# Performance work log

Measured on AMD Instinct MI355X. Metric: run time of the kernel, lower is better.

The kernel has to match this reference:

```python
import jax, jax.numpy as jnp
import numpy as np

B, N, D = 2, 512, 64
LN_EPS = 1e-5
NEG_SLOPE = 0.01  # torch nn.LeakyReLU default


def _layer_norm(x, g, b):
    m = jnp.mean(x, axis=-1, keepdims=True)
    v = jnp.mean(jnp.square(x - m), axis=-1, keepdims=True)
    return (x - m) * jax.lax.rsqrt(v + LN_EPS) * g + b


def setup_inputs() -> dict:
    key = jax.random.key(0)
    k0, k1, k2 = jax.random.split(key, 3)
    return {
        "ua": jax.random.normal(k0, (B, N, D), dtype=jnp.float32),
        "iid": jax.random.normal(k1, (B, 1, 1, D), dtype=jnp.float32),
        "ln_g": jnp.ones((D,), dtype=jnp.float32),
        "ln_b": jnp.zeros((D,), dtype=jnp.float32),
        "w_att": (jax.random.normal(k2, (3 * D, 1), dtype=jnp.float32)
                  / np.sqrt(3 * D).astype(np.float32)),
        "b_att": jnp.zeros((1,), dtype=jnp.float32),
    }


def reference(ua, iid, ln_g, ln_b, w_att, b_att):
    b, n, d = ua.shape
    # all-pairs expand: query[b,i,j,:] = ua[b,i,:], key[b,i,j,:] = ua[b,j,:]
    query = jnp.broadcast_to(ua[:, :, None, :], (b, n, n, d))
    key = jnp.broadcast_to(ua[:, None, :, :], (b, n, n, d))
    value = query * key
    iid_e = jnp.broadcast_to(iid, (b, n, n, d))
    wq = _layer_norm(query, ln_g, ln_b)
    wk = _layer_norm(key, ln_g, ln_b)
    wiid = _layer_norm(iid_e, ln_g, ln_b)
    qk = jnp.concatenate((wq, wk, wiid), axis=-1)  # [b,n,n,3d]
    qk = qk @ w_att + b_att                        # [b,n,n,1]
    qk = jax.nn.leaky_relu(qk, NEG_SLOPE)
    # dropout in eval mode -> identity
    scores = jnp.squeeze(qk, axis=-1)              # [b,n,n]
    alphas = jax.nn.softmax(scores, axis=-1)       # softmax over keys j
    alphas = jnp.broadcast_to(alphas[..., None], value.shape)
    return (alphas, value)
```

## Files before the change

kernel.cpp:

```cpp
#include <hip/hip_runtime.h>

#define BB 2
#define NN 512
#define DD 64
#define LN_EPS 1e-5f
#define NEG_SLOPE 0.01f

__device__ __forceinline__ float wave_reduce_sum(float v) {
    #pragma unroll
    for (int off = 32; off >= 1; off >>= 1)
        v += __shfl_xor(v, off, 64);
    return v;
}

__device__ __forceinline__ float wave_reduce_max(float v) {
    #pragma unroll
    for (int off = 32; off >= 1; off >>= 1)
        v = fmaxf(v, __shfl_xor(v, off, 64));
    return v;
}

__global__ __launch_bounds__(64) void precompute_kernel(
    const float* __restrict__ ua,
    const float* __restrict__ iid,
    const float* __restrict__ ln_g,
    const float* __restrict__ ln_b,
    const float* __restrict__ w_att,
    const float* __restrict__ b_att,
    float* __restrict__ sq,
    float* __restrict__ sk,
    float* __restrict__ cb) {
    const int bid = blockIdx.x;
    const int lane = threadIdx.x;

    const float g = ln_g[lane];
    const float bet = ln_b[lane];

    if (bid < BB * NN) {
        float x = ua[bid * DD + lane];
        float m = wave_reduce_sum(x) * (1.0f / DD);
        float xc = x - m;
        float var = wave_reduce_sum(xc * xc) * (1.0f / DD);
        float r = rsqrtf(var + LN_EPS);
        float w = xc * r * g + bet;
        float s1 = wave_reduce_sum(w * w_att[lane]);
        float s2 = wave_reduce_sum(w * w_att[DD + lane]);
        if (lane == 0) {
            sq[bid] = s1;
            sk[bid] = s2;
        }
    } else {
        int b = bid - BB * NN;
        float x = iid[b * DD + lane];
        float m = wave_reduce_sum(x) * (1.0f / DD);
        float xc = x - m;
        float var = wave_reduce_sum(xc * xc) * (1.0f / DD);
        float r = rsqrtf(var + LN_EPS);
        float w = xc * r * g + bet;
        float s3 = wave_reduce_sum(w * w_att[2 * DD + lane]);
        if (lane == 0) {
            cb[b] = s3 + b_att[0];
        }
    }
}

__global__ __launch_bounds__(256) void write_kernel(
    const float* __restrict__ ua,
    const float* __restrict__ sq,
    const float* __restrict__ sk,
    const float* __restrict__ cb,
    float* __restrict__ out0,
    float* __restrict__ out1) {
    __shared__ float alpha_sh[NN];
    __shared__ float red_mx[4];
    __shared__ float red_sm[4];

    const int bid = blockIdx.x;
    const int b = bid >> 9;
    const int tid = threadIdx.x;

    const float sqi = sq[bid];
    const float c = cb[b];

    float s0 = sqi + sk[b * NN + tid] + c;
    float s1 = sqi + sk[b * NN + tid + 256] + c;
    s0 = (s0 >= 0.0f) ? s0 : NEG_SLOPE * s0;
    s1 = (s1 >= 0.0f) ? s1 : NEG_SLOPE * s1;

    float mx = fmaxf(s0, s1);
    mx = wave_reduce_max(mx);
    const int wid = tid >> 6;
    if ((tid & 63) == 0) red_mx[wid] = mx;
    __syncthreads();
    mx = fmaxf(fmaxf(red_mx[0], red_mx[1]), fmaxf(red_mx[2], red_mx[3]));

    float e0 = expf(s0 - mx);
    float e1 = expf(s1 - mx);
    float sm = wave_reduce_sum(e0 + e1);
    if ((tid & 63) == 0) red_sm[wid] = sm;
    __syncthreads();
    sm = red_sm[0] + red_sm[1] + red_sm[2] + red_sm[3];
    const float inv = 1.0f / sm;

    alpha_sh[tid] = e0 * inv;
    alpha_sh[tid + 256] = e1 * inv;
    __syncthreads();

    const int d4 = tid & 15;
    const int jbase = tid >> 4;

    const float4* __restrict__ uaB = (const float4*)(ua + (size_t)b * NN * DD);
    const float4 ui = uaB[((size_t)(bid & (NN - 1))) * 16 + d4];

    float4* __restrict__ o0 = (float4*)(out0 + (size_t)bid * NN * DD);
    float4* __restrict__ o1 = (float4*)(out1 + (size_t)bid * NN * DD);

    #pragma unroll 4
    for (int k = 0; k < 32; ++k) {
        const int j = jbase + k * 16;
        const float a = alpha_sh[j];
        const float4 uj = uaB[j * 16 + d4];
        float4 av;
        av.x = a; av.y = a; av.z = a; av.w = a;
        float4 val;
        val.x = ui.x * uj.x;
        val.y = ui.y * uj.y;
        val.z = ui.z * uj.z;
        val.w = ui.w * uj.w;
        o0[j * 16 + d4] = av;
        o1[j * 16 + d4] = val;
    }
}

extern "C" void kernel_launch(void* const* d_in, const int* in_sizes, int n_in,
                              void* d_out, int out_size, void* d_ws, size_t ws_size,
                              hipStream_t stream) {
    const float* ua    = (const float*)d_in[0];
    const float* iid   = (const float*)d_in[1];
    const float* ln_g  = (const float*)d_in[2];
    const float* ln_b  = (const float*)d_in[3];
    const float* w_att = (const float*)d_in[4];
    const float* b_att = (const float*)d_in[5];

    float* out0 = (float*)d_out;
    float* out1 = out0 + (size_t)BB * NN * NN * DD;

    float* sq = (float*)d_ws;
    float* sk = sq + BB * NN;
    float* cb = sk + BB * NN;

    precompute_kernel<<<BB * NN + BB, 64, 0, stream>>>(ua, iid, ln_g, ln_b,
                                                       w_att, b_att, sq, sk, cb);
    write_kernel<<<BB * NN, 256, 0, stream>>>(ua, sq, sk, cb, out0, out1);
}
```

Before: 50.62 us.

## Split each row across two blocks and use nontemporal stores for outputs

The write kernel now launches two blocks per row, each writing half of the 512 key positions, so twice as many blocks are available to saturate the store bandwidth. Both blocks recompute the full softmax reduction, which duplicates a small amount of work. Output writes use nontemporal stores so the streamed outputs do not pollute the caches, and the vector type is switched to ext_vector_type so the multiply can be done as a single vector operation.

After: 65.76 us. 1.3x slower.

```diff
diff --git a/kernel.cpp b/kernel.cpp
--- a/kernel.cpp
+++ b/kernel.cpp
@@ -5,6 +5,8 @@
 #define DD 64
 #define LN_EPS 1e-5f
 #define NEG_SLOPE 0.01f
+
+typedef float f32x4 __attribute__((ext_vector_type(4)));
 
 __device__ __forceinline__ float wave_reduce_sum(float v) {
     #pragma unroll
@@ -71,15 +73,18 @@
     const float* __restrict__ cb,
     float* __restrict__ out0,
     float* __restrict__ out1) {
-    __shared__ float alpha_sh[NN];
+    __shared__ float alpha_sh[256];
     __shared__ float red_mx[4];
     __shared__ float red_sm[4];
 
-    const int bid = blockIdx.x;
-    const int b = bid >> 9;
+    const int bid2 = blockIdx.x;
+    const int row  = bid2 >> 1;
+    const int half = bid2 & 1;
+    const int b = row >> 9;
+    const int i = row & (NN - 1);
     const int tid = threadIdx.x;
 
-    const float sqi = sq[bid];
+    const float sqi = sq[row];
     const float c = cb[b];
 
     float s0 = sqi + sk[b * NN + tid] + c;
@@ -102,33 +107,31 @@
     sm = red_sm[0] + red_sm[1] + red_sm[2] + red_sm[3];
     const float inv = 1.0f / sm;
 
-    alpha_sh[tid] = e0 * inv;
-    alpha_sh[tid + 256] = e1 * inv;
+    alpha_sh[tid] = (half ? e1 : e0) * inv;
     __syncthreads();
 
     const int d4 = tid & 15;
     const int jbase = tid >> 4;
 
-    const float4* __restrict__ uaB = (const float4*)(ua + (size_t)b * NN * DD);
-    const float4 ui = uaB[((size_t)(bid & (NN - 1))) * 16 + d4];
+    const f32x4* __restrict__ uaB = (const f32x4*)(ua + (size_t)b * NN * DD);
+    const f32x4 ui = uaB[(size_t)i * 16 + d4];
+    const f32x4* __restrict__ uaH = uaB + (size_t)half * 256 * 16;
 
-    float4* __restrict__ o0 = (float4*)(out0 + (size_t)bid * NN * DD);
-    float4* __restrict__ o1 = (float4*)(out1 + (size_t)bid * NN * DD);
+    f32x4* __restrict__ o0 =
+        (f32x4*)(out0 + (size_t)row * NN * DD + (size_t)half * 256 * DD);
+    f32x4* __restrict__ o1 =
+        (f32x4*)(out1 + (size_t)row * NN * DD + (size_t)half * 256 * DD);
 
     #pragma unroll 4
-    for (int k = 0; k < 32; ++k) {
-        const int j = jbase + k * 16;
-        const float a = alpha_sh[j];
-        const float4 uj = uaB[j * 16 + d4];
-        float4 av;
+    for (int k = 0; k < 16; ++k) {
+        const int jl = jbase + k * 16;
+        const float a = alpha_sh[jl];
+        const f32x4 uj = uaH[jl * 16 + d4];
+        f32x4 av;
         av.x = a; av.y = a; av.z = a; av.w = a;
-        float4 val;
-        val.x = ui.x * uj.x;
-        val.y = ui.y * uj.y;
-        val.z = ui.z * uj.z;
-        val.w = ui.w * uj.w;
-        o0[j * 16 + d4] = av;
-        o1[j * 16 + d4] = val;
+        f32x4 val = ui * uj;
+        __builtin_nontemporal_store(av,  &o0[jl * 16 + d4]);
+        __builtin_nontemporal_store(val, &o1[jl * 16 + d4]);
     }
 }
 
@@ -151,5 +154,5 @@
 
     precompute_kernel<<<BB * NN + BB, 64, 0, stream>>>(ua, iid, ln_g, ln_b,
                                                        w_att, b_att, sq, sk, cb);
-    write_kernel<<<BB * NN, 256, 0, stream>>>(ua, sq, sk, cb, out0, out1);
+    write_kernel<<<BB * NN * 2, 256, 0, stream>>>(ua, sq, sk, cb, out0, out1);
 }
```

## Fuse LayerNorm score precompute into the write kernel and drop the precompute launch

Applied to the files above, without the earlier changes.

Removes the separate precompute kernel: each block recomputes the per-key LayerNorm-projected scores for its batch using folded gamma*w sums, and computes its own query score and the iid bias. The write loop now indexes contiguously by thread and uses the vector multiply, and expf becomes __expf. This removes a kernel launch and the workspace round trip. In exchange, every block redundantly re-reads all 512 rows of ua to recompute the key scores, and the variance now uses the less stable E[x^2]-m^2 formula.

After: 66.91 us. 1.32x slower.

```diff
diff --git a/kernel.cpp b/kernel.cpp
--- a/kernel.cpp
+++ b/kernel.cpp
@@ -5,6 +5,8 @@
 #define DD 64
 #define LN_EPS 1e-5f
 #define NEG_SLOPE 0.01f
+
+typedef float f32x4 __attribute__((ext_vector_type(4)));
 
 __device__ __forceinline__ float wave_reduce_sum(float v) {
     #pragma unroll
@@ -20,72 +22,90 @@
     return v;
 }
 
-__global__ __launch_bounds__(64) void precompute_kernel(
+__global__ __launch_bounds__(256) void fused_kernel(
     const float* __restrict__ ua,
     const float* __restrict__ iid,
     const float* __restrict__ ln_g,
     const float* __restrict__ ln_b,
     const float* __restrict__ w_att,
     const float* __restrict__ b_att,
-    float* __restrict__ sq,
-    float* __restrict__ sk,
-    float* __restrict__ cb) {
-    const int bid = blockIdx.x;
-    const int lane = threadIdx.x;
-
-    const float g = ln_g[lane];
-    const float bet = ln_b[lane];
-
-    if (bid < BB * NN) {
-        float x = ua[bid * DD + lane];
-        float m = wave_reduce_sum(x) * (1.0f / DD);
-        float xc = x - m;
-        float var = wave_reduce_sum(xc * xc) * (1.0f / DD);
-        float r = rsqrtf(var + LN_EPS);
-        float w = xc * r * g + bet;
-        float s1 = wave_reduce_sum(w * w_att[lane]);
-        float s2 = wave_reduce_sum(w * w_att[DD + lane]);
-        if (lane == 0) {
-            sq[bid] = s1;
-            sk[bid] = s2;
-        }
-    } else {
-        int b = bid - BB * NN;
-        float x = iid[b * DD + lane];
-        float m = wave_reduce_sum(x) * (1.0f / DD);
-        float xc = x - m;
-        float var = wave_reduce_sum(xc * xc) * (1.0f / DD);
-        float r = rsqrtf(var + LN_EPS);
-        float w = xc * r * g + bet;
-        float s3 = wave_reduce_sum(w * w_att[2 * DD + lane]);
-        if (lane == 0) {
-            cb[b] = s3 + b_att[0];
-        }
-    }
-}
-
-__global__ __launch_bounds__(256) void write_kernel(
-    const float* __restrict__ ua,
-    const float* __restrict__ sq,
-    const float* __restrict__ sk,
-    const float* __restrict__ cb,
     float* __restrict__ out0,
     float* __restrict__ out1) {
+    __shared__ f32x4 gwq_sh[DD / 4];
+    __shared__ f32x4 gwk_sh[DD / 4];
+    __shared__ float scal_sh[4];
+    __shared__ float sqc_sh[2];
     __shared__ float alpha_sh[NN];
     __shared__ float red_mx[4];
     __shared__ float red_sm[4];
 
     const int bid = blockIdx.x;
     const int b = bid >> 9;
+    const int i = bid & (NN - 1);
     const int tid = threadIdx.x;
 
-    const float sqi = sq[bid];
-    const float c = cb[b];
+    if (tid < DD) {
+        const float g  = ln_g[tid];
+        const float be = ln_b[tid];
+        const float wq = w_att[tid];
+        const float wk = w_att[DD + tid];
+        const float wi = w_att[2 * DD + tid];
+        ((float*)gwq_sh)[tid] = g * wq;
+        ((float*)gwk_sh)[tid] = g * wk;
+        const float sgq = wave_reduce_sum(g * wq);
+        const float sbq = wave_reduce_sum(be * wq);
+        const float sgk = wave_reduce_sum(g * wk);
+        const float sbk = wave_reduce_sum(be * wk);
+        const float x = iid[b * DD + tid];
+        const float m = wave_reduce_sum(x) * (1.0f / DD);
+        const float xc = x - m;
+        const float var = wave_reduce_sum(xc * xc) * (1.0f / DD);
+        const float r = rsqrtf(var + LN_EPS);
+        const float s3 = wave_reduce_sum((xc * r * g + be) * wi);
+        if (tid == 0) {
+            scal_sh[0] = sgq; scal_sh[1] = sbq;
+            scal_sh[2] = sgk; scal_sh[3] = sbk;
+            sqc_sh[1] = s3 + b_att[0];
+        }
+    }
+    __syncthreads();
 
-    float s0 = sqi + sk[b * NN + tid] + c;
-    float s1 = sqi + sk[b * NN + tid + 256] + c;
-    s0 = (s0 >= 0.0f) ? s0 : NEG_SLOPE * s0;
-    s1 = (s1 >= 0.0f) ? s1 : NEG_SLOPE * s1;
+    const float sgq = scal_sh[0], sbq = scal_sh[1];
+    const float sgk = scal_sh[2], sbk = scal_sh[3];
+
+    const f32x4* __restrict__ uaB = (const f32x4*)(ua + (size_t)b * NN * DD);
+
+    float dk0, dk1;
+    #pragma unroll
+    for (int rr = 0; rr < 2; ++rr) {
+        const int j = tid + rr * 256;
+        const f32x4* __restrict__ px = uaB + (size_t)j * 16;
+        float sx = 0.f, sxx = 0.f, axk = 0.f, axq = 0.f;
+        #pragma unroll
+        for (int k = 0; k < 16; ++k) {
+            const f32x4 x = px[k];
+            const f32x4 gk = gwk_sh[k];
+            const f32x4 gq = gwq_sh[k];
+            sx  += x.x + x.y + x.z + x.w;
+            sxx += x.x * x.x + x.y * x.y + x.z * x.z + x.w * x.w;
+            axk += x.x * gk.x + x.y * gk.y + x.z * gk.z + x.w * gk.w;
+            axq += x.x * gq.x + x.y * gq.y + x.z * gq.z + x.w * gq.w;
+        }
+        const float m = sx * (1.0f / DD);
+        const float var = sxx * (1.0f / DD) - m * m;
+        const float r = rsqrtf(var + LN_EPS);
+        const float d = r * (axk - m * sgk) + sbk;
+        if (rr == 0) dk0 = d; else dk1 = d;
+        if (j == i) sqc_sh[0] = r * (axq - m * sgq) + sbq;
+    }
+    __syncthreads();
+
+    const float sqi = sqc_sh[0];
+    const float c = sqc_sh[1];
+    float s0 = sqi + dk0 + c;
+    float s1 = sqi + dk1 + c;
+    s0 = fmaxf(s0, NEG_SLOPE * s0);
+    s1 = fmaxf(s1, NEG_SLOPE * s1);
 
     float mx = fmaxf(s0, s1);
     mx = wave_reduce_max(mx);
@@ -94,8 +114,8 @@
     __syncthreads();
     mx = fmaxf(fmaxf(red_mx[0], red_mx[1]), fmaxf(red_mx[2], red_mx[3]));
 
-    float e0 = expf(s0 - mx);
-    float e1 = expf(s1 - mx);
+    const float e0 = __expf(s0 - mx);
+    const float e1 = __expf(s1 - mx);
     float sm = wave_reduce_sum(e0 + e1);
     if ((tid & 63) == 0) red_sm[wid] = sm;
     __syncthreads();
@@ -107,28 +127,19 @@
     __syncthreads();
 
     const int d4 = tid & 15;
-    const int jbase = tid >> 4;
-
-    const float4* __restrict__ uaB = (const float4*)(ua + (size_t)b * NN * DD);
-    const float4 ui = uaB[((size_t)(bid & (NN - 1))) * 16 + d4];
-
-    float4* __restrict__ o0 = (float4*)(out0 + (size_t)bid * NN * DD);
-    float4* __restrict__ o1 = (float4*)(out1 + (size_t)bid * NN * DD);
+    const f32x4 ui = uaB[(size_t)i * 16 + d4];
+    f32x4* __restrict__ o0 = (f32x4*)(out0 + (size_t)bid * NN * DD);
+    f32x4* __restrict__ o1 = (f32x4*)(out1 + (size_t)bid * NN * DD);
 
     #pragma unroll 4
     for (int k = 0; k < 32; ++k) {
-        const int j = jbase + k * 16;
-        const float a = alpha_sh[j];
-        const float4 uj = uaB[j * 16 + d4];
-        float4 av;
+        const int idx = tid + k * 256;
+        const float a = alpha_sh[idx >> 4];
+        const f32x4 uj = uaB[idx];
+        f32x4 av;
         av.x = a; av.y = a; av.z = a; av.w = a;
-        float4 val;
-        val.x = ui.x * uj.x;
-        val.y = ui.y * uj.y;
-        val.z = ui.z * uj.z;
-        val.w = ui.w * uj.w;
-        o0[j * 16 + d4] = av;
-        o1[j * 16 + d4] = val;
+        o0[idx] = av;
+        o1[idx] = ui * uj;
     }
 }
 
@@ -145,11 +156,6 @@
     float* out0 = (float*)d_out;
     float* out1 = out0 + (size_t)BB * NN * NN * DD;
 
-    float* sq = (float*)d_ws;
-    float* sk = sq + BB * NN;
-    float* cb = sk + BB * NN;
-
-    precompute_kernel<<<BB * NN + BB, 64, 0, stream>>>(ua, iid, ln_g, ln_b,
-                                                       w_att, b_att, sq, sk, cb);
-    write_kernel<<<BB * NN, 256, 0, stream>>>(ua, sq, sk, cb, out0, out1);
+    fused_kernel<<<BB * NN, 256, 0, stream>>>(ua, iid, ln_g, ln_b,
+                                              w_att, b_att, out0, out1);
 }
```

## Fuse precompute and write kernels into one cooperative kernel with grid sync

Applied to the files above, without the earlier changes.

Merges the LayerNorm/projection precompute and the softmax/output-write kernels into one cooperative launch, using a grid-wide barrier between the two phases instead of a second kernel launch. This removes one launch and the gap between kernels. It also switches to fast __expf and a max-based leaky ReLU. The grid barrier adds its own sync cost, and the launch requires all 1024 blocks to be co-resident, which depends on occupancy. The workload is dominated by writing 64 MB of output, so the saving can only be small.

After: 95.76 us. +89.2%, slower.

```diff
diff --git a/kernel.cpp b/kernel.cpp
--- a/kernel.cpp
+++ b/kernel.cpp
@@ -1,10 +1,15 @@
 #include <hip/hip_runtime.h>
+#include <hip/hip_cooperative_groups.h>
+
+namespace cg = cooperative_groups;
 
 #define BB 2
 #define NN 512
 #define DD 64
 #define LN_EPS 1e-5f
 #define NEG_SLOPE 0.01f
+
+typedef float f32x4 __attribute__((ext_vector_type(4)));
 
 __device__ __forceinline__ float wave_reduce_sum(float v) {
     #pragma unroll
@@ -20,7 +25,7 @@
     return v;
 }
 
-__global__ __launch_bounds__(64) void precompute_kernel(
+__global__ __launch_bounds__(256, 4) void fused_coop_kernel(
     const float* __restrict__ ua,
     const float* __restrict__ iid,
     const float* __restrict__ ln_g,
@@ -29,14 +34,22 @@
     const float* __restrict__ b_att,
     float* __restrict__ sq,
     float* __restrict__ sk,
-    float* __restrict__ cb) {
+    float* __restrict__ cb,
+    float* __restrict__ out0,
+    float* __restrict__ out1) {
+    __shared__ float alpha_sh[NN];
+    __shared__ float red_mx[4];
+    __shared__ float red_sm[4];
+
     const int bid = blockIdx.x;
-    const int lane = threadIdx.x;
+    const int b = bid >> 9;
+    const int i = bid & (NN - 1);
+    const int tid = threadIdx.x;
 
-    const float g = ln_g[lane];
-    const float bet = ln_b[lane];
-
-    if (bid < BB * NN) {
+    if (tid < 64) {
+        const int lane = tid;
+        const float g = ln_g[lane];
+        const float bet = ln_b[lane];
         float x = ua[bid * DD + lane];
         float m = wave_reduce_sum(x) * (1.0f / DD);
         float xc = x - m;
@@ -49,8 +62,10 @@
             sq[bid] = s1;
             sk[bid] = s2;
         }
-    } else {
-        int b = bid - BB * NN;
+    } else if (i == 0 && tid < 128) {
+        const int lane = tid - 64;
+        const float g = ln_g[lane];
+        const float bet = ln_b[lane];
         float x = iid[b * DD + lane];
         float m = wave_reduce_sum(x) * (1.0f / DD);
         float xc = x - m;
@@ -62,30 +77,16 @@
             cb[b] = s3 + b_att[0];
         }
     }
-}
 
-__global__ __launch_bounds__(256) void write_kernel(
-    const float* __restrict__ ua,
-    const float* __restrict__ sq,
-    const float* __restrict__ sk,
-    const float* __restrict__ cb,
-    float* __restrict__ out0,
-    float* __restrict__ out1) {
-    __shared__ float alpha_sh[NN];
-    __shared__ float red_mx[4];
-    __shared__ float red_sm[4];
-
-    const int bid = blockIdx.x;
-    const int b = bid >> 9;
-    const int tid = threadIdx.x;
+    cg::this_grid().sync();
 
     const float sqi = sq[bid];
     const float c = cb[b];
 
     float s0 = sqi + sk[b * NN + tid] + c;
     float s1 = sqi + sk[b * NN + tid + 256] + c;
-    s0 = (s0 >= 0.0f) ? s0 : NEG_SLOPE * s0;
-    s1 = (s1 >= 0.0f) ? s1 : NEG_SLOPE * s1;
+    s0 = fmaxf(s0, NEG_SLOPE * s0);
+    s1 = fmaxf(s1, NEG_SLOPE * s1);
 
     float mx = fmaxf(s0, s1);
     mx = wave_reduce_max(mx);
@@ -94,8 +95,8 @@
     __syncthreads();
     mx = fmaxf(fmaxf(red_mx[0], red_mx[1]), fmaxf(red_mx[2], red_mx[3]));
 
-    float e0 = expf(s0 - mx);
-    float e1 = expf(s1 - mx);
+    const float e0 = __expf(s0 - mx);
+    const float e1 = __expf(s1 - mx);
     float sm = wave_reduce_sum(e0 + e1);
     if ((tid & 63) == 0) red_sm[wid] = sm;
     __syncthreads();
@@ -106,29 +107,21 @@
     alpha_sh[tid + 256] = e1 * inv;
     __syncthreads();
 
-    const int d4 = tid & 15;
-    const int jbase = tid >> 4;
+    const f32x4* __restrict__ uaB = (const f32x4*)(ua + (size_t)b * NN * DD);
+    const f32x4 ui = uaB[(size_t)i * 16 + (tid & 15)];
 
-    const float4* __restrict__ uaB = (const float4*)(ua + (size_t)b * NN * DD);
-    const float4 ui = uaB[((size_t)(bid & (NN - 1))) * 16 + d4];
-
-    float4* __restrict__ o0 = (float4*)(out0 + (size_t)bid * NN * DD);
-    float4* __restrict__ o1 = (float4*)(out1 + (size_t)bid * NN * DD);
+    f32x4* __restrict__ o0 = (f32x4*)(out0 + (size_t)bid * NN * DD);
+    f32x4* __restrict__ o1 = (f32x4*)(out1 + (size_t)bid * NN * DD);
 
     #pragma unroll 4
     for (int k = 0; k < 32; ++k) {
-        const int j = jbase + k * 16;
-        const float a = alpha_sh[j];
-        const float4 uj = uaB[j * 16 + d4];
-        float4 av;
+        const int idx = tid + k * 256;
+        const float a = alpha_sh[idx >> 4];
+        const f32x4 uj = uaB[idx];
+        f32x4 av;
         av.x = a; av.y = a; av.z = a; av.w = a;
-        float4 val;
-        val.x = ui.x * uj.x;
-        val.y = ui.y * uj.y;
-        val.z = ui.z * uj.z;
-        val.w = ui.w * uj.w;
-        o0[j * 16 + d4] = av;
-        o1[j * 16 + d4] = val;
+        o0[idx] = av;
+        o1[idx] = ui * uj;
     }
 }
 
@@ -149,7 +142,12 @@
     float* sk = sq + BB * NN;
     float* cb = sk + BB * NN;
 
-    precompute_kernel<<<BB * NN + BB, 64, 0, stream>>>(ua, iid, ln_g, ln_b,
-                                                       w_att, b_att, sq, sk, cb);
-    write_kernel<<<BB * NN, 256, 0, stream>>>(ua, sq, sk, cb, out0, out1);
+    void* args[] = {
+        (void*)&ua, (void*)&iid, (void*)&ln_g, (void*)&ln_b,
+        (void*)&w_att, (void*)&b_att,
+        (void*)&sq, (void*)&sk, (void*)&cb,
+        (void*)&out0, (void*)&out1,
+    };
+    hipLaunchCooperativeKernel((const void*)fused_coop_kernel,
+                               dim3(BB * NN), dim3(256), args, 0, stream);
 }
```
